# Performance work log

Measured on AMD Instinct MI355X. Metric: run time of the kernel, lower is better.

## Reference

```python
import jax, jax.numpy as jnp
import numpy as np
import math

D_MODEL = 1024
NUM_HEADS = 16
HEAD_DIM = D_MODEL // NUM_HEADS  # 64
THETA = 10000.0
BATCH = 2
SEQ = 2048


def setup_inputs() -> dict:
    key = jax.random.key(0)
    ks = jax.random.split(key, 5)
    scale = 0.02
    return {
        "in_features": jax.random.normal(ks[0], (BATCH, SEQ, D_MODEL), jnp.float32),
        "q_proj": jax.random.normal(ks[1], (D_MODEL, D_MODEL), jnp.float32) * scale,
        "k_proj": jax.random.normal(ks[2], (D_MODEL, D_MODEL), jnp.float32) * scale,
        "v_proj": jax.random.normal(ks[3], (D_MODEL, D_MODEL), jnp.float32) * scale,
        "o_proj": jax.random.normal(ks[4], (D_MODEL, D_MODEL), jnp.float32) * scale,
        "token_positions": jnp.arange(SEQ, dtype=jnp.int32),
    }


def _rope(x, token_positions):
    # x: [b, h, s, head_dim]; interleaved even/odd rotation
    half = HEAD_DIM // 2
    inv_freq = 1.0 / (THETA ** (2.0 * jnp.arange(half, dtype=x.dtype) / HEAD_DIM))
    angle = token_positions.astype(x.dtype)[:, None] * inv_freq[None, :]  # [s, half]
    cos, sin = jnp.cos(angle), jnp.sin(angle)
    x_e, x_o = x[..., ::2], x[..., 1::2]
    r_e = x_e * cos - x_o * sin
    r_o = x_e * sin + x_o * cos
    # interleave back: [..., s, half, 2] -> [..., s, head_dim]
    return jnp.stack([r_e, r_o], axis=-1).reshape(x.shape)


def reference(in_features, q_proj, k_proj, v_proj, o_proj, token_positions):
    b, s, _ = in_features.shape
    # projections: weight layout is [d_out, d_in]
    Q = jnp.einsum('bsd,kd->bsk', in_features, q_proj)
    K = jnp.einsum('bsd,kd->bsk', in_features, k_proj)
    V = jnp.einsum('bsd,kd->bsk', in_features, v_proj)
    # split heads: [b, h, s, head_dim]
    Q = Q.reshape(b, s, NUM_HEADS, HEAD_DIM).transpose(0, 2, 1, 3)
    K = K.reshape(b, s, NUM_HEADS, HEAD_DIM).transpose(0, 2, 1, 3)
    V = V.reshape(b, s, NUM_HEADS, HEAD_DIM).transpose(0, 2, 1, 3)
    Q = _rope(Q, token_positions)
    K = _rope(K, token_positions)
    scores = jnp.einsum('bhnd,bhmd->bhnm', Q, K) / math.sqrt(HEAD_DIM)
    causal = jnp.tril(jnp.ones((s, s), dtype=bool))  # [s, s]
    scores = jnp.where(causal[None, None], scores, -jnp.inf)
    attn = jax.nn.softmax(scores, axis=-1)
    out = jnp.einsum('bhnm,bhmd->bhnd', attn, V)
    out = out.transpose(0, 2, 1, 3).reshape(b, s, D_MODEL)
    return jnp.einsum('bsv,dv->bsd', out, o_proj)
```

## Files before the change

### kernel.cpp

```cpp
#include <hip/hip_runtime.h>
#include <hip/hip_bf16.h>

#define D_MODEL 1024
#define NHEAD   16
#define HDIM    64
#define SEQQ    2048
#define NBATCH  2
#define MROWS   (NBATCH * SEQQ)

typedef unsigned short u16;
typedef __attribute__((ext_vector_type(8))) short short8;
typedef __attribute__((ext_vector_type(4))) short bf16x4;
typedef __attribute__((ext_vector_type(4))) float floatx4;

__device__ __forceinline__ u16 f2b(float f) {
    union { __hip_bfloat16 h; u16 u; } cv;
    cv.h = __float2bfloat16(f);
    return cv.u;
}
__device__ __forceinline__ float b2f(u16 u) {
    return __uint_as_float(((unsigned int)u) << 16);
}
__device__ __forceinline__ short8 load8(const u16* p) {
    return *reinterpret_cast<const short8*>(p);
}
__device__ __forceinline__ bf16x4 load4v(const u16* p) {
    return *reinterpret_cast<const bf16x4*>(p);
}
__device__ __forceinline__ unsigned pack2(float lo, float hi) {
    return ((unsigned)f2b(hi) << 16) | (unsigned)f2b(lo);
}
__device__ __forceinline__ void async_cp16(const void* g, void* l) {
    __builtin_amdgcn_global_load_lds(
        (const __attribute__((address_space(1))) void*)g,
        (__attribute__((address_space(3))) void*)l, 16, 0, 0);
}

__global__ void cvt_all(const float* __restrict__ X,
                        const float* __restrict__ w0, const float* __restrict__ w1,
                        const float* __restrict__ w2, const float* __restrict__ w3,
                        const int* __restrict__ pos,
                        u16* __restrict__ xo,
                        u16* __restrict__ o0, u16* __restrict__ o1,
                        u16* __restrict__ o2, u16* __restrict__ o3,
                        float2* __restrict__ tab) {
    const int z = blockIdx.y;
    const int i = blockIdx.x * 256 + threadIdx.x;
    if (z == 8) {
        if (i < SEQQ * 32) {
            const int j = i >> 11, s = i & (SEQQ - 1);
            const float p = (float)pos[s];
            const float inv = expf(-(float)j * (9.210340371976184f / 32.0f));
            float sn, cs;
            sincosf(p * inv, &sn, &cs);
            tab[i] = make_float2(cs, sn);
        }
        return;
    }
    const int n4 = (D_MODEL * D_MODEL) / 4;
    const float* in;
    u16* out;
    if (z < 4) { in = X + (size_t)z * n4 * 4;  out = xo + (size_t)z * n4 * 4; }
    else {
        in  = (z == 4) ? w0 : (z == 5) ? w1 : (z == 6) ? w2 : w3;
        out = (z == 4) ? o0 : (z == 5) ? o1 : (z == 6) ? o2 : o3;
    }
    int src = i;
    if (z == 4 || z == 5) {
        const int orow = i >> 8;
        const int g    = i & 255;
        const int irow = (orow & ~63) | (((orow & 31) << 1) | ((orow >> 5) & 1));
        src = irow * 256 + g;
    }
    float4 v = reinterpret_cast<const float4*>(in)[src];
    ushort4 o;
    o.x = f2b(v.x); o.y = f2b(v.y); o.z = f2b(v.z); o.w = f2b(v.w);
    reinterpret_cast<ushort4*>(out)[i] = o;
}

__global__ __launch_bounds__(256, 6) void gemm_qkv(
    const u16* __restrict__ A,
    const u16* __restrict__ B0, const u16* __restrict__ B1, const u16* __restrict__ B2,
    u16* __restrict__ Qt, u16* __restrict__ Kt, u16* __restrict__ Vt,
    const float2* __restrict__ tab)
{
    const int K = D_MODEL;
    const int z = blockIdx.z;
    const u16* Bt = (z == 0) ? B0 : (z == 1 ? B1 : B2);

    __shared__ __attribute__((aligned(16))) u16 As[2][64 * 32];
    __shared__ __attribute__((aligned(16))) u16 Bs[2][128 * 32];

    const int tid  = threadIdx.x;
    const int w    = tid >> 6;
    const int lane = tid & 63;
    const int l15  = lane & 15;
    const int quad = lane >> 4;
    const int wm   = w >> 1, wn = w & 1;
    const int tm   = blockIdx.x * 64, tn = blockIdx.y * 128;

    floatx4 acc[2][4];
#pragma unroll
    for (int i = 0; i < 2; i++)
#pragma unroll
        for (int j = 0; j < 4; j++) {
            floatx4 zz = {0.f, 0.f, 0.f, 0.f};
            acc[i][j] = zz;
        }

    const int srow = lane >> 2;
    const int scol = (lane & 3) * 8;

    auto stage = [&](int buf, int k0) {
#pragma unroll
        for (int ch = w; ch < 12; ch += 4) {
            if (ch < 4) async_cp16(A  + (size_t)(tm + ch * 16 + srow) * K + k0 + scol,
                                   &As[buf][ch * 512]);
            else        async_cp16(Bt + (size_t)(tn + (ch - 4) * 16 + srow) * K + k0 + scol,
                                   &Bs[buf][(ch - 4) * 512]);
        }
    };

    stage(0, 0);

    for (int kt = 0; kt < 32; ++kt) {
        asm volatile("s_waitcnt vmcnt(0)" ::: "memory");
        __builtin_amdgcn_s_barrier();
        if (kt < 31) stage((kt + 1) & 1, (kt + 1) * 32);

        const u16* AsB = &As[kt & 1][0];
        const u16* BsB = &Bs[kt & 1][0];

        short8 af[2], bfr[4];
#pragma unroll
        for (int mi = 0; mi < 2; mi++)
            af[mi] = load8(&AsB[(wm * 32 + mi * 16 + l15) * 32 + quad * 8]);
#pragma unroll
        for (int ni = 0; ni < 4; ni++)
            bfr[ni] = load8(&BsB[(wn * 64 + ni * 16 + l15) * 32 + quad * 8]);
#pragma unroll
        for (int mi = 0; mi < 2; mi++)
#pragma unroll
            for (int ni = 0; ni < 4; ni++)
                acc[mi][ni] = __builtin_amdgcn_mfma_f32_16x16x32_bf16(af[mi], bfr[ni], acc[mi][ni], 0, 0, 0);
    }

    if (z == 2) {
#pragma unroll
        for (int mi = 0; mi < 2; mi++) {
            const int r0 = tm + wm * 32 + mi * 16 + quad * 4;
            const int bb = r0 >> 11, s0 = r0 & (SEQQ - 1);
#pragma unroll
            for (int ni = 0; ni < 4; ni++) {
                const int colb = tn + wn * 64 + ni * 16 + l15;
                const int d = colb & 63, hh = colb >> 6;
                ushort4 pk;
                pk.x = f2b(acc[mi][ni][0]);
                pk.y = f2b(acc[mi][ni][1]);
                pk.z = f2b(acc[mi][ni][2]);
                pk.w = f2b(acc[mi][ni][3]);
                *reinterpret_cast<ushort4*>(
                    &Vt[(((size_t)(bb * NHEAD + hh)) * HDIM + d) * SEQQ + s0]) = pk;
            }
        }
    } else {
        const float qsc = (z == 0) ? 0.18033688011112042f : 1.0f;
        u16* Outp = (z == 0) ? Qt : Kt;
        const int hh = (tn >> 6) + wn;
        float4 ta[2], tb[2];
        auto ldtab = [&](int g) {
            const int mi = g >> 1, ni = g & 1;
            const int qq = ni * 16 + l15;
            const int s0 = (tm + wm * 32 + mi * 16 + quad * 4) & (SEQQ - 1);
            ta[g & 1] = *reinterpret_cast<const float4*>(&tab[qq * SEQQ + s0]);
            tb[g & 1] = *reinterpret_cast<const float4*>(&tab[qq * SEQQ + s0 + 2]);
        };
        ldtab(0);
#pragma unroll
        for (int g = 0; g < 4; ++g) {
            if (g < 3) ldtab(g + 1);
            const int mi = g >> 1, ni = g & 1;
            const int qq = ni * 16 + l15;
            const int r0 = tm + wm * 32 + mi * 16 + quad * 4;
            const int bb = r0 >> 11, s0 = r0 & (SEQQ - 1);
            const float4 A4 = ta[g & 1], B4 = tb[g & 1];
            const float cs[4] = {A4.x, A4.z, B4.x, B4.z};
            const float sn[4] = {A4.y, A4.w, B4.y, B4.w};
#pragma unroll
            for (int rg = 0; rg < 4; rg++) {
                const float e = acc[mi][ni][rg];
                const float o = acc[mi][ni + 2][rg];
                const unsigned val =
                    (unsigned)f2b((e * cs[rg] - o * sn[rg]) * qsc) |
                    ((unsigned)f2b((e * sn[rg] + o * cs[rg]) * qsc) << 16);
                *reinterpret_cast<unsigned*>(
                    &Outp[(((size_t)(bb * NHEAD + hh)) * SEQQ + (s0 + rg)) * HDIM + 2 * qq]) = val;
            }
        }
    }
}

__global__ __launch_bounds__(256, 4) void attn_kernel(
    const u16* __restrict__ Qt, const u16* __restrict__ Kt, const u16* __restrict__ Vt,
    u16* __restrict__ Out)
{
    const int bid = blockIdx.x;
    const int xcd = bid & 7;
    const int u   = bid >> 3;
    const int col = xcd * 4 + (u & 3);
    const int m   = u >> 2;
    int qsub;
    if      (m < 8)  qsub = 31 - m;
    else if (m < 16) qsub = m - 8;
    else if (m < 24) qsub = 39 - m;
    else             qsub = m - 16;
    const int h = col & (NHEAD - 1), b = col >> 4;

    const int tid = threadIdx.x, w = tid >> 6, lane = tid & 63;
    const int l15 = lane & 15, quad = lane >> 4;
    const size_t bh = (size_t)(b * NHEAD + h);
    const u16* Qh = Qt + bh * SEQQ * HDIM;
    const u16* Kh = Kt + bh * SEQQ * HDIM;
    const u16* Vh = Vt + bh * HDIM * SEQQ;

    __shared__ __attribute__((aligned(16))) u16 Ks[2][64 * 64];
    __shared__ __attribute__((aligned(16))) u16 Vs[2][64 * 64];

    short8 ones;
#pragma unroll
    for (int i = 0; i < 8; i++) ones[i] = (short)0x3F80;

    const int rr  = lane >> 3;
    const int swz = ((lane & 7) ^ rr) * 8;
    auto stage = [&](int buf, int tt) {
        const int k0s = tt * 64;
        async_cp16(Kh + (size_t)(k0s + w * 8 + rr) * HDIM + swz,       &Ks[buf][w * 512]);
        async_cp16(Kh + (size_t)(k0s + (w + 4) * 8 + rr) * HDIM + swz, &Ks[buf][(w + 4) * 512]);
        async_cp16(Vh + (size_t)(w * 8 + rr) * SEQQ + k0s + swz,       &Vs[buf][w * 512]);
        async_cp16(Vh + (size_t)((w + 4) * 8 + rr) * SEQQ + k0s + swz, &Vs[buf][(w + 4) * 512]);
    };

    const int s7  = l15 & 7;
    const int sw1 = ((quad)     ^ s7) * 8;
    const int sw2 = ((quad + 4) ^ s7) * 8;
    const int vo0 = (((quad >> 1)    ) ^ s7) * 8 + (quad & 1) * 4;
    const int vo1 = (((quad >> 1) + 2) ^ s7) * 8 + (quad & 1) * 4;
    const int vo2 = (((quad >> 1) + 4) ^ s7) * 8 + (quad & 1) * 4;
    const int vo3 = (((quad >> 1) + 6) ^ s7) * 8 + (quad & 1) * 4;

    const int q0w   = qsub * 64 + w * 16;
    const int tmaxp = qsub;

    short8 qf[2];
#pragma unroll
    for (int kk = 0; kk < 2; kk++)
        qf[kk] = load8(&Qh[(size_t)(q0w + l15) * HDIM + kk * 32 + quad * 8]);

    floatx4 O[4];
    floatx4 l_acc = {0.f, 0.f, 0.f, 0.f};
#pragma unroll
    for (int c = 0; c < 4; c++) { floatx4 zz = {0.f, 0.f, 0.f, 0.f}; O[c] = zz; }

    stage(0, 0);

    for (int t = 0; t <= tmaxp; ++t) {
        asm volatile("s_waitcnt vmcnt(0)" ::: "memory");
        __builtin_amdgcn_s_barrier();
        if (t < tmaxp) stage((t + 1) & 1, t + 1);

        const u16* KsB = &Ks[t & 1][0];
        const u16* VsB = &Vs[t & 1][0];
        const int k0 = t * 64;

        floatx4 S[4];
        __builtin_amdgcn_s_setprio(1);
#pragma unroll
        for (int c = 0; c < 4; c++) {
            const int rowb = (c * 16 + l15) * 64;
            floatx4 zz = {0.f, 0.f, 0.f, 0.f};
            S[c] = __builtin_amdgcn_mfma_f32_16x16x32_bf16(load8(&KsB[rowb + sw1]), qf[0], zz,   0, 0, 0);
            S[c] = __builtin_amdgcn_mfma_f32_16x16x32_bf16(load8(&KsB[rowb + sw2]), qf[1], S[c], 0, 0, 0);
        }
        __builtin_amdgcn_s_setprio(0);

        if (t == tmaxp) {
            const int q = q0w + l15;
#pragma unroll
            for (int c = 0; c < 4; c++)
#pragma unroll
                for (int r = 0; r < 4; r++)
                    if (k0 + c * 16 + quad * 4 + r > q) S[c][r] = -1e30f;
        }

#pragma unroll
        for (int c = 0; c < 4; c++)
#pragma unroll
            for (int r = 0; r < 4; r++)
                S[c][r] = __builtin_amdgcn_exp2f(S[c][r]);

        union { short8 v; unsigned u[4]; } pf0, pf1;
        pf0.u[0] = pack2(S[0][0], S[0][1]);
        pf0.u[1] = pack2(S[0][2], S[0][3]);
        pf0.u[2] = pack2(S[1][0], S[1][1]);
        pf0.u[3] = pack2(S[1][2], S[1][3]);
        pf1.u[0] = pack2(S[2][0], S[2][1]);
        pf1.u[1] = pack2(S[2][2], S[2][3]);
        pf1.u[2] = pack2(S[3][0], S[3][1]);
        pf1.u[3] = pack2(S[3][2], S[3][3]);

        __builtin_amdgcn_s_setprio(1);
        l_acc = __builtin_amdgcn_mfma_f32_16x16x32_bf16(pf0.v, ones, l_acc, 0, 0, 0);
        l_acc = __builtin_amdgcn_mfma_f32_16x16x32_bf16(pf1.v, ones, l_acc, 0, 0, 0);

#pragma unroll
        for (int c2 = 0; c2 < 4; c2++) {
            const int rowb = (c2 * 16 + l15) * 64;
            bf16x4 a0 = load4v(&VsB[rowb + vo0]);
            bf16x4 a1 = load4v(&VsB[rowb + vo1]);
            bf16x4 a2 = load4v(&VsB[rowb + vo2]);
            bf16x4 a3 = load4v(&VsB[rowb + vo3]);
            short8 v0 = __builtin_shufflevector(a0, a1, 0, 1, 2, 3, 4, 5, 6, 7);
            short8 v1 = __builtin_shufflevector(a2, a3, 0, 1, 2, 3, 4, 5, 6, 7);
            O[c2] = __builtin_amdgcn_mfma_f32_16x16x32_bf16(pf0.v, v0, O[c2], 0, 0, 0);
            O[c2] = __builtin_amdgcn_mfma_f32_16x16x32_bf16(pf1.v, v1, O[c2], 0, 0, 0);
        }
        __builtin_amdgcn_s_setprio(0);
    }

    float inv_l[4];
#pragma unroll
    for (int r = 0; r < 4; r++) inv_l[r] = 1.0f / l_acc[r];

#pragma unroll
    for (int c2 = 0; c2 < 4; c2++)
#pragma unroll
        for (int r = 0; r < 4; r++) {
            const int q    = q0w + quad * 4 + r;
            const int colo = h * HDIM + c2 * 16 + l15;
            Out[(size_t)(b * SEQQ + q) * D_MODEL + colo] = f2b(O[c2][r] * inv_l[r]);
        }
}

__global__ __launch_bounds__(256) void gemm_o(
    const u16* __restrict__ A, const u16* __restrict__ Bt, float* __restrict__ C)
{
    const int K = D_MODEL, N = D_MODEL;
    __shared__ __attribute__((aligned(16))) u16 As[3][64 * 32];
    __shared__ __attribute__((aligned(16))) u16 Bs[3][64 * 32];

    const int tid  = threadIdx.x;
    const int w    = tid >> 6;
    const int lane = tid & 63;
    const int l15  = lane & 15;
    const int quad = lane >> 4;
    const int wm   = w >> 1, wn = w & 1;
    const int tm   = blockIdx.x * 64, tn = blockIdx.y * 64;

    floatx4 acc[2][2];
#pragma unroll
    for (int i = 0; i < 2; i++)
#pragma unroll
        for (int j = 0; j < 2; j++) {
            floatx4 z = {0.f, 0.f, 0.f, 0.f};
            acc[i][j] = z;
        }

    const int srow = lane >> 2;
    const int scol = (lane & 3) * 8;

    auto stage = [&](int buf, int k0) {
        async_cp16(A  + (size_t)(tm + w * 16 + srow) * K + k0 + scol, &As[buf][w * 512]);
        async_cp16(Bt + (size_t)(tn + w * 16 + srow) * K + k0 + scol, &Bs[buf][w * 512]);
    };

    stage(0, 0);
    stage(1, 32);

    for (int kt = 0; kt < 32; ++kt) {
        if (kt < 30) asm volatile("s_waitcnt vmcnt(2)" ::: "memory");
        else         asm volatile("s_waitcnt vmcnt(0)" ::: "memory");
        __builtin_amdgcn_s_barrier();
        if (kt < 30) stage((kt + 2) % 3, (kt + 2) * 32);

        const u16* AsB = &As[kt % 3][0];
        const u16* BsB = &Bs[kt % 3][0];

        short8 af[2], bfr[2];
#pragma unroll
        for (int mi = 0; mi < 2; mi++)
            af[mi] = load8(&AsB[(wm * 32 + mi * 16 + l15) * 32 + quad * 8]);
#pragma unroll
        for (int ni = 0; ni < 2; ni++)
            bfr[ni] = load8(&BsB[(wn * 32 + ni * 16 + l15) * 32 + quad * 8]);
#pragma unroll
        for (int mi = 0; mi < 2; mi++)
#pragma unroll
            for (int ni = 0; ni < 2; ni++)
                acc[mi][ni] = __builtin_amdgcn_mfma_f32_16x16x32_bf16(af[mi], bfr[ni], acc[mi][ni], 0, 0, 0);
    }

#pragma unroll
    for (int mi = 0; mi < 2; mi++)
#pragma unroll
        for (int ni = 0; ni < 2; ni++)
#pragma unroll
            for (int rg = 0; rg < 4; rg++) {
                int row = tm + wm * 32 + mi * 16 + quad * 4 + rg;
                int col = tn + wn * 32 + ni * 16 + l15;
                C[(size_t)row * N + col] = acc[mi][ni][rg];
            }
}

extern "C" void kernel_launch(void* const* d_in, const int* in_sizes, int n_in,
                              void* d_out, int out_size, void* d_ws, size_t ws_size,
                              hipStream_t stream)
{
    const float* X  = (const float*)d_in[0];
    const float* Wq = (const float*)d_in[1];
    const float* Wk = (const float*)d_in[2];
    const float* Wv = (const float*)d_in[3];
    const float* Wo = (const float*)d_in[4];
    const int* tpos = (const int*)d_in[5];
    float* out = (float*)d_out;
    char* ws = (char*)d_ws;

    const size_t MB = (size_t)1 << 20;
    u16*    Xb  = (u16*)(ws + 0);
    u16*    WqB = (u16*)(ws + 8 * MB);
    u16*    WkB = (u16*)(ws + 10 * MB);
    u16*    WvB = (u16*)(ws + 12 * MB);
    u16*    WoB = (u16*)(ws + 14 * MB);
    float2* tab = (float2*)(ws + 16 * MB);
    u16*    Qt  = (u16*)(ws + 24 * MB);
    u16*    Kt  = (u16*)(ws + 32 * MB);
    u16*    Vt  = (u16*)(ws + 40 * MB);
    u16*   AOut = (u16*)(ws + 48 * MB);

    cvt_all<<<dim3(1024, 9), 256, 0, stream>>>(X, Wq, Wk, Wv, Wo, tpos,
                                               Xb, WqB, WkB, WvB, WoB, tab);

    gemm_qkv<<<dim3(64, 8, 3), 256, 0, stream>>>(Xb, WqB, WkB, WvB,
                                                 Qt, Kt, Vt, tab);
    attn_kernel<<<dim3(1024, 1, 1), 256, 0, stream>>>(Qt, Kt, Vt, AOut);
    gemm_o<<<dim3(64, 16), 256, 0, stream>>>(AOut, WoB, out);
}
```

Baseline: 186.1 us.

## Fuse Q, K, V projections into one block sharing the staged A tile

Each QKV GEMM block now computes all three projections for its 64x128 tile, loading the activation tile once and staging three weight tiles, instead of launching a separate z-slice per projection. This removes redundant activation loads. In exchange the grid shrinks from 1536 to 512 blocks, the accumulators triple (96 floats per thread), and shared memory grows, so launch bounds drop occupancy to 2 blocks per SM. There may also be tail or parallelism loss on a chip with many CUs.

```diff
diff --git a/kernel.cpp b/kernel.cpp
--- a/kernel.cpp
+++ b/kernel.cpp
@@ -78,18 +78,16 @@
     reinterpret_cast<ushort4*>(out)[i] = o;
 }
 
-__global__ __launch_bounds__(256, 6) void gemm_qkv(
+__global__ __launch_bounds__(256, 2) void gemm_qkv(
     const u16* __restrict__ A,
     const u16* __restrict__ B0, const u16* __restrict__ B1, const u16* __restrict__ B2,
     u16* __restrict__ Qt, u16* __restrict__ Kt, u16* __restrict__ Vt,
     const float2* __restrict__ tab)
 {
     const int K = D_MODEL;
-    const int z = blockIdx.z;
-    const u16* Bt = (z == 0) ? B0 : (z == 1 ? B1 : B2);
 
     __shared__ __attribute__((aligned(16))) u16 As[2][64 * 32];
-    __shared__ __attribute__((aligned(16))) u16 Bs[2][128 * 32];
+    __shared__ __attribute__((aligned(16))) u16 Bs[2][3][128 * 32];
 
     const int tid  = threadIdx.x;
     const int w    = tid >> 6;
@@ -99,25 +97,27 @@
     const int wm   = w >> 1, wn = w & 1;
     const int tm   = blockIdx.x * 64, tn = blockIdx.y * 128;
 
-    floatx4 acc[2][4];
-#pragma unroll
-    for (int i = 0; i < 2; i++)
-#pragma unroll
-        for (int j = 0; j < 4; j++) {
-            floatx4 zz = {0.f, 0.f, 0.f, 0.f};
-            acc[i][j] = zz;
-        }
+    floatx4 acc[3][2][4];
+#pragma unroll
+    for (int zz = 0; zz < 3; zz++)
+#pragma unroll
+        for (int i = 0; i < 2; i++)
+#pragma unroll
+            for (int j = 0; j < 4; j++) {
+                floatx4 z4 = {0.f, 0.f, 0.f, 0.f};
+                acc[zz][i][j] = z4;
+            }
 
     const int srow = lane >> 2;
     const int scol = (lane & 3) * 8;
 
     auto stage = [&](int buf, int k0) {
-#pragma unroll
-        for (int ch = w; ch < 12; ch += 4) {
-            if (ch < 4) async_cp16(A  + (size_t)(tm + ch * 16 + srow) * K + k0 + scol,
-                                   &As[buf][ch * 512]);
-            else        async_cp16(Bt + (size_t)(tn + (ch - 4) * 16 + srow) * K + k0 + scol,
-                                   &Bs[buf][(ch - 4) * 512]);
+        async_cp16(A + (size_t)(tm + w * 16 + srow) * K + k0 + scol, &As[buf][w * 512]);
+#pragma unroll
+        for (int ch = w; ch < 8; ch += 4) {
+            async_cp16(B0 + (size_t)(tn + ch * 16 + srow) * K + k0 + scol, &Bs[buf][0][ch * 512]);
+            async_cp16(B1 + (size_t)(tn + ch * 16 + srow) * K + k0 + scol, &Bs[buf][1][ch * 512]);
+            async_cp16(B2 + (size_t)(tn + ch * 16 + srow) * K + k0 + scol, &Bs[buf][2][ch * 512]);
         }
     };
 
@@ -128,45 +128,50 @@
         __builtin_amdgcn_s_barrier();
         if (kt < 31) stage((kt + 1) & 1, (kt + 1) * 32);
 
-        const u16* AsB = &As[kt & 1][0];
-        const u16* BsB = &Bs[kt & 1][0];
-
-        short8 af[2], bfr[4];
+        const int buf = kt & 1;
+        short8 af[2];
 #pragma unroll
         for (int mi = 0; mi < 2; mi++)
-            af[mi] = load8(&AsB[(wm * 32 + mi * 16 + l15) * 32 + quad * 8]);
-#pragma unroll
-        for (int ni = 0; ni < 4; ni++)
-            bfr[ni] = load8(&BsB[(wn * 64 + ni * 16 + l15) * 32 + quad * 8]);
-#pragma unroll
-        for (int mi = 0; mi < 2; mi++)
+            af[mi] = load8(&As[buf][(wm * 32 + mi * 16 + l15) * 32 + quad * 8]);
+
+#pragma unroll
+        for (int zz = 0; zz < 3; zz++) {
+            short8 bfr[4];
 #pragma unroll
             for (int ni = 0; ni < 4; ni++)
-                acc[mi][ni] = __builtin_amdgcn_mfma_f32_16x16x32_bf16(af[mi], bfr[ni], acc[mi][ni], 0, 0, 0);
-    }
-
-    if (z == 2) {
-#pragma unroll
-        for (int mi = 0; mi < 2; mi++) {
-            const int r0 = tm + wm * 32 + mi * 16 + quad * 4;
-            const int bb = r0 >> 11, s0 = r0 & (SEQQ - 1);
-#pragma unroll
-            for (int ni = 0; ni < 4; ni++) {
-                const int colb = tn + wn * 64 + ni * 16 + l15;
-                const int d = colb & 63, hh = colb >> 6;
-                ushort4 pk;
-                pk.x = f2b(acc[mi][ni][0]);
-                pk.y = f2b(acc[mi][ni][1]);
-                pk.z = f2b(acc[mi][ni][2]);
-                pk.w = f2b(acc[mi][ni][3]);
-                *reinterpret_cast<ushort4*>(
-                    &Vt[(((size_t)(bb * NHEAD + hh)) * HDIM + d) * SEQQ + s0]) = pk;
-            }
-        }
-    } else {
-        const float qsc = (z == 0) ? 0.18033688011112042f : 1.0f;
-        u16* Outp = (z == 0) ? Qt : Kt;
-        const int hh = (tn >> 6) + wn;
+                bfr[ni] = load8(&Bs[buf][zz][(wn * 64 + ni * 16 + l15) * 32 + quad * 8]);
+#pragma unroll
+            for (int mi = 0; mi < 2; mi++)
+#pragma unroll
+                for (int ni = 0; ni < 4; ni++)
+                    acc[zz][mi][ni] = __builtin_amdgcn_mfma_f32_16x16x32_bf16(
+                        af[mi], bfr[ni], acc[zz][mi][ni], 0, 0, 0);
+        }
+    }
+
+#pragma unroll
+    for (int mi = 0; mi < 2; mi++) {
+        const int r0 = tm + wm * 32 + mi * 16 + quad * 4;
+        const int bb = r0 >> 11, s0 = r0 & (SEQQ - 1);
+#pragma unroll
+        for (int ni = 0; ni < 4; ni++) {
+            const int colb = tn + wn * 64 + ni * 16 + l15;
+            const int d = colb & 63, hh = colb >> 6;
+            ushort4 pk;
+            pk.x = f2b(acc[2][mi][ni][0]);
+            pk.y = f2b(acc[2][mi][ni][1]);
+            pk.z = f2b(acc[2][mi][ni][2]);
+            pk.w = f2b(acc[2][mi][ni][3]);
+            *reinterpret_cast<ushort4*>(
+                &Vt[(((size_t)(bb * NHEAD + hh)) * HDIM + d) * SEQQ + s0]) = pk;
+        }
+    }
+
+    const int hh = (tn >> 6) + wn;
+#pragma unroll
+    for (int zz = 0; zz < 2; zz++) {
+        const float qsc = (zz == 0) ? 0.18033688011112042f : 1.0f;
+        u16* Outp = (zz == 0) ? Qt : Kt;
         float4 ta[2], tb[2];
         auto ldtab = [&](int g) {
             const int mi = g >> 1, ni = g & 1;
@@ -188,8 +193,8 @@
             const float sn[4] = {A4.y, A4.w, B4.y, B4.w};
 #pragma unroll
             for (int rg = 0; rg < 4; rg++) {
-                const float e = acc[mi][ni][rg];
-                const float o = acc[mi][ni + 2][rg];
+                const float e = acc[zz][mi][ni][rg];
+                const float o = acc[zz][mi][ni + 2][rg];
                 const unsigned val =
                     (unsigned)f2b((e * cs[rg] - o * sn[rg]) * qsc) |
                     ((unsigned)f2b((e * sn[rg] + o * cs[rg]) * qsc) << 16);
@@ -439,8 +444,8 @@
     cvt_all<<<dim3(1024, 9), 256, 0, stream>>>(X, Wq, Wk, Wv, Wo, tpos,
                                                Xb, WqB, WkB, WvB, WoB, tab);
 
-    gemm_qkv<<<dim3(64, 8, 3), 256, 0, stream>>>(Xb, WqB, WkB, WvB,
-                                                 Qt, Kt, Vt, tab);
+    gemm_qkv<<<dim3(64, 8), 256, 0, stream>>>(Xb, WqB, WkB, WvB,
+                                              Qt, Kt, Vt, tab);
     attn_kernel<<<dim3(1024, 1, 1), 256, 0, stream>>>(Qt, Kt, Vt, AOut);
     gemm_o<<<dim3(64, 16), 256, 0, stream>>>(AOut, WoB, out);
 }
```

Result: no change. 183.9 us (-1.2%).

## Enlarge QKV GEMM tiles to 256x256 with 8 waves and 4-stage async pipeline

Applied to the files above, without the earlier changes.

The fused QKV projection GEMM now uses 256x256 output tiles per 512-thread block, with 8 waves each computing 128x64. Operands are staged through a 4-slot LDS ring filled three half-K steps ahead, with partial vmcnt waits. MFMA issue runs under raised wave priority. This is meant to cut global and LDS traffic per FLOP and hide load latency better. The cost is far fewer blocks (192, below the CU count), about 128KB of LDS per block and a high register load from 32 accumulator tiles.

```diff
diff --git a/kernel.cpp b/kernel.cpp
--- a/kernel.cpp
+++ b/kernel.cpp
@@ -78,7 +78,7 @@
     reinterpret_cast<ushort4*>(out)[i] = o;
 }
 
-__global__ __launch_bounds__(256, 6) void gemm_qkv(
+__global__ __launch_bounds__(512, 2) void gemm_qkv(
     const u16* __restrict__ A,
     const u16* __restrict__ B0, const u16* __restrict__ B1, const u16* __restrict__ B2,
     u16* __restrict__ Qt, u16* __restrict__ Kt, u16* __restrict__ Vt,
@@ -88,77 +88,86 @@
     const int z = blockIdx.z;
     const u16* Bt = (z == 0) ? B0 : (z == 1 ? B1 : B2);
 
-    __shared__ __attribute__((aligned(16))) u16 As[2][64 * 32];
-    __shared__ __attribute__((aligned(16))) u16 Bs[2][128 * 32];
+    __shared__ __attribute__((aligned(16))) u16 As[4][256 * 32];
+    __shared__ __attribute__((aligned(16))) u16 Bs[4][256 * 32];
 
     const int tid  = threadIdx.x;
     const int w    = tid >> 6;
     const int lane = tid & 63;
     const int l15  = lane & 15;
     const int quad = lane >> 4;
-    const int wm   = w >> 1, wn = w & 1;
-    const int tm   = blockIdx.x * 64, tn = blockIdx.y * 128;
-
-    floatx4 acc[2][4];
-#pragma unroll
-    for (int i = 0; i < 2; i++)
-#pragma unroll
-        for (int j = 0; j < 4; j++) {
-            floatx4 zz = {0.f, 0.f, 0.f, 0.f};
-            acc[i][j] = zz;
+    const int wr   = w >> 2;
+    const int wc   = w & 3;
+    const int tm   = blockIdx.x * 256, tn = blockIdx.y * 256;
+
+    floatx4 acc[8][4];
+#pragma unroll
+    for (int m = 0; m < 8; m++)
+#pragma unroll
+        for (int n = 0; n < 4; n++) {
+            floatx4 z4 = {0.f, 0.f, 0.f, 0.f};
+            acc[m][n] = z4;
         }
 
     const int srow = lane >> 2;
-    const int scol = (lane & 3) * 8;
-
-    auto stage = [&](int buf, int k0) {
-#pragma unroll
-        for (int ch = w; ch < 12; ch += 4) {
-            if (ch < 4) async_cp16(A  + (size_t)(tm + ch * 16 + srow) * K + k0 + scol,
-                                   &As[buf][ch * 512]);
-            else        async_cp16(Bt + (size_t)(tn + (ch - 4) * 16 + srow) * K + k0 + scol,
-                                   &Bs[buf][(ch - 4) * 512]);
-        }
+    const int sc8  = (lane & 3) * 8;
+    auto stageH = [&](int hh) {
+        const int kb = (hh >> 1) * 64 + (hh & 1) * 32;
+        const int sl = hh & 3;
+        const int r0 = w * 32 + srow;
+        async_cp16(A  + (size_t)(tm + r0) * K + kb + sc8,      &As[sl][(w * 32) * 32]);
+        async_cp16(A  + (size_t)(tm + r0 + 16) * K + kb + sc8, &As[sl][(w * 32 + 16) * 32]);
+        async_cp16(Bt + (size_t)(tn + r0) * K + kb + sc8,      &Bs[sl][(w * 32) * 32]);
+        async_cp16(Bt + (size_t)(tn + r0 + 16) * K + kb + sc8, &Bs[sl][(w * 32 + 16) * 32]);
     };
 
-    stage(0, 0);
-
-    for (int kt = 0; kt < 32; ++kt) {
-        asm volatile("s_waitcnt vmcnt(0)" ::: "memory");
+    stageH(0); stageH(1); stageH(2);
+    asm volatile("s_waitcnt vmcnt(8)" ::: "memory");
+    __builtin_amdgcn_s_barrier();
+
+    for (int q = 0; q < 32; ++q) {
+        if (q + 3 < 32) stageH(q + 3);
+
+        const u16* Aslot = &As[q & 3][0];
+        const u16* Bslot = &Bs[q & 3][0];
+        short8 af[8], bf[4];
+#pragma unroll
+        for (int m = 0; m < 8; m++)
+            af[m] = load8(&Aslot[(wr * 128 + m * 16 + l15) * 32 + quad * 8]);
+#pragma unroll
+        for (int n = 0; n < 4; n++)
+            bf[n] = load8(&Bslot[(wc * 64 + n * 16 + l15) * 32 + quad * 8]);
+
+        if (q <= 28)      asm volatile("s_waitcnt vmcnt(8)" ::: "memory");
+        else if (q == 29) asm volatile("s_waitcnt vmcnt(4)" ::: "memory");
+        else              asm volatile("s_waitcnt vmcnt(0)" ::: "memory");
         __builtin_amdgcn_s_barrier();
-        if (kt < 31) stage((kt + 1) & 1, (kt + 1) * 32);
-
-        const u16* AsB = &As[kt & 1][0];
-        const u16* BsB = &Bs[kt & 1][0];
-
-        short8 af[2], bfr[4];
-#pragma unroll
-        for (int mi = 0; mi < 2; mi++)
-            af[mi] = load8(&AsB[(wm * 32 + mi * 16 + l15) * 32 + quad * 8]);
-#pragma unroll
-        for (int ni = 0; ni < 4; ni++)
-            bfr[ni] = load8(&BsB[(wn * 64 + ni * 16 + l15) * 32 + quad * 8]);
-#pragma unroll
-        for (int mi = 0; mi < 2; mi++)
-#pragma unroll
-            for (int ni = 0; ni < 4; ni++)
-                acc[mi][ni] = __builtin_amdgcn_mfma_f32_16x16x32_bf16(af[mi], bfr[ni], acc[mi][ni], 0, 0, 0);
-    }
+
+        __builtin_amdgcn_s_setprio(1);
+#pragma unroll
+        for (int m = 0; m < 8; m++)
+#pragma unroll
+            for (int n = 0; n < 4; n++)
+                acc[m][n] = __builtin_amdgcn_mfma_f32_16x16x32_bf16(af[m], bf[n], acc[m][n], 0, 0, 0);
+        __builtin_amdgcn_s_setprio(0);
+        __builtin_amdgcn_s_barrier();
+    }
+
+    const int hh = (tn >> 6) + wc;
 
     if (z == 2) {
 #pragma unroll
-        for (int mi = 0; mi < 2; mi++) {
-            const int r0 = tm + wm * 32 + mi * 16 + quad * 4;
+        for (int m = 0; m < 8; m++) {
+            const int r0 = tm + wr * 128 + m * 16 + quad * 4;
             const int bb = r0 >> 11, s0 = r0 & (SEQQ - 1);
 #pragma unroll
-            for (int ni = 0; ni < 4; ni++) {
-                const int colb = tn + wn * 64 + ni * 16 + l15;
-                const int d = colb & 63, hh = colb >> 6;
+            for (int n = 0; n < 4; n++) {
+                const int d = n * 16 + l15;
                 ushort4 pk;
-                pk.x = f2b(acc[mi][ni][0]);
-                pk.y = f2b(acc[mi][ni][1]);
-                pk.z = f2b(acc[mi][ni][2]);
-                pk.w = f2b(acc[mi][ni][3]);
+                pk.x = f2b(acc[m][n][0]);
+                pk.y = f2b(acc[m][n][1]);
+                pk.z = f2b(acc[m][n][2]);
+                pk.w = f2b(acc[m][n][3]);
                 *reinterpret_cast<ushort4*>(
                     &Vt[(((size_t)(bb * NHEAD + hh)) * HDIM + d) * SEQQ + s0]) = pk;
             }
@@ -166,35 +175,34 @@
     } else {
         const float qsc = (z == 0) ? 0.18033688011112042f : 1.0f;
         u16* Outp = (z == 0) ? Qt : Kt;
-        const int hh = (tn >> 6) + wn;
         float4 ta[2], tb[2];
         auto ldtab = [&](int g) {
-            const int mi = g >> 1, ni = g & 1;
-            const int qq = ni * 16 + l15;
-            const int s0 = (tm + wm * 32 + mi * 16 + quad * 4) & (SEQQ - 1);
+            const int m = g >> 1, n = g & 1;
+            const int qq = n * 16 + l15;
+            const int s0 = (tm + wr * 128 + m * 16 + quad * 4) & (SEQQ - 1);
             ta[g & 1] = *reinterpret_cast<const float4*>(&tab[qq * SEQQ + s0]);
             tb[g & 1] = *reinterpret_cast<const float4*>(&tab[qq * SEQQ + s0 + 2]);
         };
         ldtab(0);
 #pragma unroll
-        for (int g = 0; g < 4; ++g) {
-            if (g < 3) ldtab(g + 1);
-            const int mi = g >> 1, ni = g & 1;
-            const int qq = ni * 16 + l15;
-            const int r0 = tm + wm * 32 + mi * 16 + quad * 4;
+        for (int g = 0; g < 16; ++g) {
+            if (g < 15) ldtab(g + 1);
+            const int m = g >> 1, n = g & 1;
+            const int qq = n * 16 + l15;
+            const int r0 = tm + wr * 128 + m * 16 + quad * 4;
             const int bb = r0 >> 11, s0 = r0 & (SEQQ - 1);
             const float4 A4 = ta[g & 1], B4 = tb[g & 1];
             const float cs[4] = {A4.x, A4.z, B4.x, B4.z};
             const float sn[4] = {A4.y, A4.w, B4.y, B4.w};
 #pragma unroll
-            for (int rg = 0; rg < 4; rg++) {
-                const float e = acc[mi][ni][rg];
-                const float o = acc[mi][ni + 2][rg];
+            for (int j = 0; j < 4; j++) {
+                const float e = acc[m][n][j];
+                const float o = acc[m][n + 2][j];
                 const unsigned val =
-                    (unsigned)f2b((e * cs[rg] - o * sn[rg]) * qsc) |
-                    ((unsigned)f2b((e * sn[rg] + o * cs[rg]) * qsc) << 16);
+                    (unsigned)f2b((e * cs[j] - o * sn[j]) * qsc) |
+                    ((unsigned)f2b((e * sn[j] + o * cs[j]) * qsc) << 16);
                 *reinterpret_cast<unsigned*>(
-                    &Outp[(((size_t)(bb * NHEAD + hh)) * SEQQ + (s0 + rg)) * HDIM + 2 * qq]) = val;
+                    &Outp[(((size_t)(bb * NHEAD + hh)) * SEQQ + (s0 + j)) * HDIM + 2 * qq]) = val;
             }
         }
     }
@@ -439,7 +447,7 @@
     cvt_all<<<dim3(1024, 9), 256, 0, stream>>>(X, Wq, Wk, Wv, Wo, tpos,
                                                Xb, WqB, WkB, WvB, WoB, tab);
 
-    gemm_qkv<<<dim3(64, 8, 3), 256, 0, stream>>>(Xb, WqB, WkB, WvB,
+    gemm_qkv<<<dim3(16, 4, 3), 512, 0, stream>>>(Xb, WqB, WkB, WvB,
                                                  Qt, Kt, Vt, tab);
     attn_kernel<<<dim3(1024, 1, 1), 256, 0, stream>>>(Qt, Kt, Vt, AOut);
     gemm_o<<<dim3(64, 16), 256, 0, stream>>>(AOut, WoB, out);
```

Measured after the change: 192.5 us. 3.4% more time.
